# Kernel tuning notes

Measured on AMD Instinct MI355X. Metric: run time of the kernel, lower is better.

Reference implementation:

```python
import jax, jax.numpy as jnp
import numpy as np

DIM = 384
B = 256
EPS = 1e-5


def _conv_replicate(x, W, pad):
    # x: [B,C,H,W], W: [O,I,kh,kw]; replicate (edge) padding then VALID conv
    x = jnp.pad(x, ((0, 0), (0, 0), (pad, pad), (pad, pad)), mode='edge')
    return jax.lax.conv_general_dilated(
        x, W, window_strides=(1, 1), padding='VALID',
        dimension_numbers=('NCHW', 'OIHW', 'NCHW'))


def _bn(x, g, b, m, v):
    scale = (g / jnp.sqrt(v + EPS))[None, :, None, None]
    return (x - m[None, :, None, None]) * scale + b[None, :, None, None]


def _clip_features(target, bbox):
    # target: [B, 576, C] -> vectorized per-sample crop + nearest resize to 12x12
    bb = bbox * 24.0
    x, y, w, h = bb[:, 0], bb[:, 1], bb[:, 2], bb[:, 3]
    l = (w + h) / 2
    l = jnp.sqrt((w + l) * (h + l))
    x_min = jnp.clip(jnp.ceil(x - l / 2), 0, 23).astype(jnp.int32)
    y_min = jnp.clip(jnp.ceil(y - l / 2), 0, 23).astype(jnp.int32)
    x_max = jnp.clip(jnp.trunc(x + l / 2), 0, 23).astype(jnp.int32)
    y_max = jnp.clip(jnp.trunc(y + l / 2), 0, 23).astype(jnp.int32)
    i12 = jnp.arange(12, dtype=jnp.int32)
    # nearest-neighbor source index: crop_start + floor(i * crop_size / 12)
    rows = y_min[:, None] + (i12[None, :] * (y_max - y_min)[:, None]) // 12  # [B,12]
    cols = x_min[:, None] + (i12[None, :] * (x_max - x_min)[:, None]) // 12  # [B,12]
    rows = jnp.clip(rows, 0, 23)
    cols = jnp.clip(cols, 0, 23)
    Bn, N, C = target.shape
    tflat = jnp.transpose(target, (0, 2, 1))  # [B, C, 576] (row-major 24x24)
    idx = rows[:, :, None] * 24 + cols[:, None, :]  # [B,12,12]
    idx = jnp.broadcast_to(idx.reshape(Bn, 1, 144), (Bn, C, 144))
    out = jnp.take_along_axis(tflat, idx, axis=2)  # [B, C, 144]
    return out.reshape(Bn, C, 12, 12)


def setup_inputs() -> dict:
    key = jax.random.key(0)
    ks = jax.random.split(key, 8)
    temp = jax.random.normal(ks[0], (B, 144, DIM), dtype=jnp.float32)
    target = jax.random.normal(ks[1], (B, 576, DIM), dtype=jnp.float32)
    u = jax.random.uniform(ks[2], (B, 4), dtype=jnp.float32)
    # centers in [0.3,0.7], sizes in [0.25,0.45] -> always a valid non-empty crop
    bbox = jnp.concatenate([0.3 + 0.4 * u[:, :2], 0.25 + 0.2 * u[:, 2:]], axis=1)
    W1 = jax.random.normal(ks[3], (DIM, DIM, 5, 5), dtype=jnp.float32) * 0.02
    W2 = jax.random.normal(ks[4], (DIM, DIM, 3, 3), dtype=jnp.float32) * 0.05
    g1 = jnp.ones((DIM,), jnp.float32)
    b1 = jnp.zeros((DIM,), jnp.float32)
    m1 = jax.random.normal(ks[5], (DIM,), dtype=jnp.float32) * 0.1
    v1 = jnp.ones((DIM,), jnp.float32)
    g2 = jnp.ones((DIM,), jnp.float32)
    b2 = jnp.zeros((DIM,), jnp.float32)
    m2 = jax.random.normal(ks[6], (DIM,), dtype=jnp.float32) * 0.1
    v2 = jnp.ones((DIM,), jnp.float32)
    return dict(temp=temp, target=target, bbox=bbox, W1=W1, g1=g1, b1=b1,
                m1=m1, v1=v1, W2=W2, g2=g2, b2=b2, m2=m2, v2=v2)


def reference(temp, target, bbox, W1, g1, b1, m1, v1, W2, g2, b2, m2, v2):
    ta = _clip_features(target, bbox)  # [B, C, 12, 12]
    h1 = jax.nn.leaky_relu(_bn(_conv_replicate(ta, W1, 2), g1, b1, m1, v1), 0.01)
    h2 = jax.nn.leaky_relu(_bn(_conv_replicate(h1, W2, 1), g2, b2, m2, v2), 0.01)
    Bn, N, C = temp.shape
    t = jnp.transpose(temp, (0, 2, 1)).reshape(Bn, C, 12, 12)
    out = (t + h2).reshape(Bn, C, 144)
    return jnp.transpose(out, (0, 2, 1))  # [B, 144, C]
```

## Files before the change

### kernel.cpp

```cpp
#include <hip/hip_runtime.h>
#include <math.h>

#define NBATCH 256
#define CDIM   384

typedef __attribute__((ext_vector_type(4))) float  f32x4;
typedef __attribute__((ext_vector_type(8))) __bf16 bf16x8;
typedef __attribute__((ext_vector_type(4))) __bf16 bf16x4;

__device__ __forceinline__ void load16(const void* g, void* l) {
    __builtin_amdgcn_global_load_lds(
        (const __attribute__((address_space(1))) void*)g,
        (__attribute__((address_space(3))) void*)l, 16, 0, 0);
}

__global__ __launch_bounds__(256) void gather_bf16(
    const float* __restrict__ target,
    const float* __restrict__ bbox,
    __bf16* __restrict__ ta)
{
    const int b = blockIdx.x, t = threadIdx.x;
    __shared__ int pos[144];

    if (t < 144) {
        const float bx0 = bbox[b * 4 + 0] * 24.f;
        const float by0 = bbox[b * 4 + 1] * 24.f;
        const float bw  = bbox[b * 4 + 2] * 24.f;
        const float bh  = bbox[b * 4 + 3] * 24.f;
        const float l0 = (bw + bh) * 0.5f;
        const float l  = sqrtf((bw + l0) * (bh + l0));
        const int xmin = (int)fminf(fmaxf(ceilf (bx0 - l * 0.5f), 0.f), 23.f);
        const int ymin = (int)fminf(fmaxf(ceilf (by0 - l * 0.5f), 0.f), 23.f);
        const int xmax = (int)fminf(fmaxf(truncf(bx0 + l * 0.5f), 0.f), 23.f);
        const int ymax = (int)fminf(fmaxf(truncf(by0 + l * 0.5f), 0.f), 23.f);
        const int i = t / 12, j = t % 12;
        int r = ymin + (i * (ymax - ymin)) / 12;
        int c = xmin + (j * (xmax - xmin)) / 12;
        r = min(max(r, 0), 23);
        c = min(max(c, 0), 23);
        pos[t] = r * 24 + c;
    }
    __syncthreads();

    const float* tb  = target + (size_t)b * 576 * 384;
    __bf16*      tab = ta     + (size_t)b * 144 * 384;
    for (int idx = t; idx < 144 * 96; idx += 256) {
        const int p = idx / 96, c4 = idx - p * 96;
        const float4 v = *(const float4*)&tb[(size_t)pos[p] * 384 + c4 * 4];
        bf16x4 o = { (__bf16)v.x, (__bf16)v.y, (__bf16)v.z, (__bf16)v.w };
        *(bf16x4*)&tab[(size_t)p * 384 + c4 * 4] = o;
    }
}

template <int TAPS>
__global__ __launch_bounds__(256) void prep_w(
    const float* __restrict__ W, __bf16* __restrict__ Wt)
{
    const int K = TAPS * 384;
    __shared__ float ws[TAPS * 384];
    const int oc = blockIdx.x;
    const float* src = W + (size_t)oc * K;
    for (int i = threadIdx.x; i < K; i += 256) ws[i] = src[i];
    __syncthreads();
    __bf16* dst = Wt + (size_t)oc * K;
    for (int i = threadIdx.x; i < K; i += 256) {
        const int tap = i / 384;
        const int ic  = i - tap * 384;
        dst[i] = (__bf16)ws[ic * TAPS + tap];
    }
}

template <int TAPS, int KW, int PAD, bool RESID>
__global__ __launch_bounds__(256, 3) void conv_mfma(
    const __bf16* __restrict__ A,
    const __bf16* __restrict__ Wt,
    const float* __restrict__ gg, const float* __restrict__ bb,
    const float* __restrict__ mm, const float* __restrict__ vv,
    const float* __restrict__ temp,
    void* __restrict__ outp)
{
    const int K  = TAPS * 384;
    const int IT = TAPS * 12;
    const int m0 = blockIdx.x * 128;
    const int n0 = blockIdx.y * 128;
    const int t  = threadIdx.x;
    const int lane  = t & 63, w = t >> 6;
    const int wm    = (w & 1) * 64, wn = (w >> 1) * 64;
    const int col16 = lane & 15,  quad = lane >> 4;

    __shared__ __bf16 As0[128 * 32], As1[128 * 32], As2[128 * 32];
    __shared__ __bf16 Bs0[128 * 32], Bs1[128 * 32], Bs2[128 * 32];

    const int r0   = t >> 2, slot = t & 3;
    const int kg   = slot ^ ((r0 >> 1) & 3);
    const int mrow0 = m0 + r0, mrow1 = m0 + r0 + 64;
    const int b0 = mrow0 / 144, p0 = mrow0 - b0 * 144;
    const int b1 = mrow1 / 144, p1 = mrow1 - b1 * 144;
    const int y0 = p0 / 12, x0 = p0 - y0 * 12;
    const int y1 = p1 / 12, x1 = p1 - y1 * 12;
    const __bf16* Ab0 = A + (size_t)b0 * 144 * 384 + kg * 8;
    const __bf16* Ab1 = A + (size_t)b1 * 144 * 384 + kg * 8;

    int offA[4], offB[4];
#pragma unroll
    for (int mi = 0; mi < 4; ++mi) {
        const int r = wm + mi * 16 + col16;
        offA[mi] = r * 32 + (quad ^ ((r >> 1) & 3)) * 8;
    }
#pragma unroll
    for (int ni = 0; ni < 4; ++ni) {
        const int r = wn + ni * 16 + col16;
        offB[ni] = r * 32 + (quad ^ ((r >> 1) & 3)) * 8;
    }

    f32x4 acc[4][4];
#pragma unroll
    for (int mi = 0; mi < 4; ++mi)
#pragma unroll
        for (int ni = 0; ni < 4; ++ni)
            acc[mi][ni] = (f32x4){0.f, 0.f, 0.f, 0.f};

    int jn = 0, tapn = 0, next = 0;
    const __bf16* aT0;
    const __bf16* aT1;
    {
        const int sy0 = min(max(y0 - PAD, 0), 11), sx0 = min(max(x0 - PAD, 0), 11);
        const int sy1 = min(max(y1 - PAD, 0), 11), sx1 = min(max(x1 - PAD, 0), 11);
        aT0 = Ab0 + (size_t)(sy0 * 12 + sx0) * 384;
        aT1 = Ab1 + (size_t)(sy1 * 12 + sx1) * 384;
    }
    const __bf16* bT0 = Wt + (size_t)(n0 + r0)      * K + kg * 8;
    const __bf16* bT1 = Wt + (size_t)(n0 + r0 + 64) * K + kg * 8;

    auto issue = [&](__bf16* SA, __bf16* SB) {
        load16(aT0 + jn * 32, &SA[t * 8]);
        load16(aT1 + jn * 32, &SA[(t + 256) * 8]);
        load16(bT0 + jn * 32, &SB[t * 8]);
        load16(bT1 + jn * 32, &SB[(t + 256) * 8]);
    };
    auto advance = [&]() {
        if (++jn == 12) {
            jn = 0;
            ++tapn;
            if (tapn < TAPS) {
                const int ky = tapn / KW - PAD, kx = tapn % KW - PAD;
                const int sy0 = min(max(y0 + ky, 0), 11), sx0 = min(max(x0 + kx, 0), 11);
                const int sy1 = min(max(y1 + ky, 0), 11), sx1 = min(max(x1 + kx, 0), 11);
                aT0 = Ab0 + (size_t)(sy0 * 12 + sx0) * 384;
                aT1 = Ab1 + (size_t)(sy1 * 12 + sx1) * 384;
                bT0 += 384;
                bT1 += 384;
            }
        }
    };
    auto step = [&](const __bf16* SA, const __bf16* SB,
                    __bf16* NA, __bf16* NB_, bool last) {
        if (last) asm volatile("s_waitcnt vmcnt(0)" ::: "memory");
        else      asm volatile("s_waitcnt vmcnt(4)" ::: "memory");
        __builtin_amdgcn_s_barrier();
        __builtin_amdgcn_sched_barrier(0);
        if (next < IT) { issue(NA, NB_); advance(); ++next; }
        bf16x8 av[4], bv[4];
#pragma unroll
        for (int mi = 0; mi < 4; ++mi) av[mi] = *(const bf16x8*)&SA[offA[mi]];
#pragma unroll
        for (int ni = 0; ni < 4; ++ni) bv[ni] = *(const bf16x8*)&SB[offB[ni]];
        __builtin_amdgcn_s_setprio(1);
#pragma unroll
        for (int mi = 0; mi < 4; ++mi)
#pragma unroll
            for (int ni = 0; ni < 4; ++ni)
                acc[mi][ni] = __builtin_amdgcn_mfma_f32_16x16x32_bf16(
                    av[mi], bv[ni], acc[mi][ni], 0, 0, 0);
        __builtin_amdgcn_s_setprio(0);
    };

    issue(As0, Bs0); advance(); ++next;
    issue(As1, Bs1); advance(); ++next;

    for (int it3 = 0; it3 < IT; it3 += 3) {
        step(As0, Bs0, As2, Bs2, it3 + 1 == IT);
        step(As1, Bs1, As0, Bs0, it3 + 2 == IT);
        step(As2, Bs2, As1, Bs1, it3 + 3 == IT);
    }

#pragma unroll
    for (int ni = 0; ni < 4; ++ni) {
        const int gn = n0 + wn + ni * 16 + col16;
        const float scale = gg[gn] * rsqrtf(vv[gn] + 1e-5f);
        const float shift = bb[gn] - mm[gn] * scale;
        if (!RESID) {
            __bf16* h1 = (__bf16*)outp;
#pragma unroll
            for (int mi = 0; mi < 4; ++mi) {
                const int gm = m0 + wm + mi * 16 + quad * 4;
#pragma unroll
                for (int r = 0; r < 4; ++r) {
                    float v = acc[mi][ni][r] * scale + shift;
                    v = (v >= 0.f) ? v : 0.01f * v;
                    h1[(size_t)(gm + r) * 384 + gn] = (__bf16)v;
                }
            }
        } else {
            float* outF = (float*)outp;
#pragma unroll
            for (int mi = 0; mi < 4; ++mi) {
                const int gm = m0 + wm + mi * 16 + quad * 4;
#pragma unroll
                for (int r = 0; r < 4; ++r) {
                    float v = acc[mi][ni][r] * scale + shift;
                    v = (v >= 0.f) ? v : 0.01f * v;
                    outF[(size_t)(gm + r) * 384 + gn] =
                        temp[(size_t)(gm + r) * 384 + gn] + v;
                }
            }
        }
    }
}

extern "C" void kernel_launch(void* const* d_in, const int* in_sizes, int n_in,
                              void* d_out, int out_size, void* d_ws, size_t ws_size,
                              hipStream_t stream) {
    const float* temp   = (const float*)d_in[0];
    const float* target = (const float*)d_in[1];
    const float* bbox   = (const float*)d_in[2];
    const float* W1     = (const float*)d_in[3];
    const float* g1     = (const float*)d_in[4];
    const float* b1     = (const float*)d_in[5];
    const float* m1     = (const float*)d_in[6];
    const float* v1     = (const float*)d_in[7];
    const float* W2     = (const float*)d_in[8];
    const float* g2     = (const float*)d_in[9];
    const float* b2     = (const float*)d_in[10];
    const float* m2     = (const float*)d_in[11];
    const float* v2     = (const float*)d_in[12];
    float* out = (float*)d_out;

    __bf16* ta  = (__bf16*)d_ws;
    __bf16* h1  = ta  + (size_t)NBATCH * 144 * CDIM;
    __bf16* Wt1 = h1  + (size_t)NBATCH * 144 * CDIM;
    __bf16* Wt2 = Wt1 + (size_t)CDIM * 25 * CDIM;

    prep_w<25><<<dim3(CDIM), dim3(256), 0, stream>>>(W1, Wt1);
    prep_w<9><<<dim3(CDIM), dim3(256), 0, stream>>>(W2, Wt2);
    gather_bf16<<<dim3(NBATCH), dim3(256), 0, stream>>>(target, bbox, ta);

    conv_mfma<25, 5, 2, false><<<dim3(288, 3), dim3(256), 0, stream>>>(
        ta, Wt1, g1, b1, m1, v1, nullptr, (void*)h1);
    conv_mfma<9, 3, 1, true><<<dim3(288, 3), dim3(256), 0, stream>>>(
        h1, Wt2, g2, b2, m2, v2, temp, (void*)out);
}
```

Baseline: 835.4 us.

## Enlarge conv GEMM tile to 256x128 and remap blocks for XCD locality

Each block of the implicit-GEMM convolutions now computes a 256x128 output tile instead of 128x128. Each wave holds an 8x4 grid of MFMA accumulators, so more MFMAs run per LDS byte loaded and per barrier. A linear block index is also permuted so that consecutive work items land on the same XCD, which should improve L2 reuse of the A and weight tiles. The cost is higher register and LDS use (occupancy hint lowered to 2 blocks per SIMD) and half as many blocks (432), which may leave the 256 CUs less evenly loaded.

```diff
diff --git a/kernel.cpp b/kernel.cpp
--- a/kernel.cpp
+++ b/kernel.cpp
@@ -71,7 +71,7 @@
 }
 
 template <int TAPS, int KW, int PAD, bool RESID>
-__global__ __launch_bounds__(256, 3) void conv_mfma(
+__global__ __launch_bounds__(256, 2) void conv_mfma(
     const __bf16* __restrict__ A,
     const __bf16* __restrict__ Wt,
     const float* __restrict__ gg, const float* __restrict__ bb,
@@ -81,29 +81,38 @@
 {
     const int K  = TAPS * 384;
     const int IT = TAPS * 12;
-    const int m0 = blockIdx.x * 128;
-    const int n0 = blockIdx.y * 128;
+
+    const int l    = blockIdx.x + 144 * blockIdx.y;
+    const int work = (l & 7) * 54 + (l >> 3);
+    const int wx   = work % 144, wy = work / 144;
+    const int m0   = wx * 256;
+    const int n0   = wy * 128;
+
     const int t  = threadIdx.x;
     const int lane  = t & 63, w = t >> 6;
-    const int wm    = (w & 1) * 64, wn = (w >> 1) * 64;
+    const int wm    = (w & 1) * 128, wn = (w >> 1) * 64;
     const int col16 = lane & 15,  quad = lane >> 4;
 
-    __shared__ __bf16 As0[128 * 32], As1[128 * 32], As2[128 * 32];
+    __shared__ __bf16 As0[256 * 32], As1[256 * 32], As2[256 * 32];
     __shared__ __bf16 Bs0[128 * 32], Bs1[128 * 32], Bs2[128 * 32];
 
     const int r0   = t >> 2, slot = t & 3;
     const int kg   = slot ^ ((r0 >> 1) & 3);
-    const int mrow0 = m0 + r0, mrow1 = m0 + r0 + 64;
-    const int b0 = mrow0 / 144, p0 = mrow0 - b0 * 144;
-    const int b1 = mrow1 / 144, p1 = mrow1 - b1 * 144;
-    const int y0 = p0 / 12, x0 = p0 - y0 * 12;
-    const int y1 = p1 / 12, x1 = p1 - y1 * 12;
-    const __bf16* Ab0 = A + (size_t)b0 * 144 * 384 + kg * 8;
-    const __bf16* Ab1 = A + (size_t)b1 * 144 * 384 + kg * 8;
-
-    int offA[4], offB[4];
-#pragma unroll
-    for (int mi = 0; mi < 4; ++mi) {
+
+    int yq[4], xq[4];
+    const __bf16* Abq[4];
+#pragma unroll
+    for (int q = 0; q < 4; ++q) {
+        const int mrow = m0 + r0 + 64 * q;
+        const int b = mrow / 144, p = mrow - b * 144;
+        yq[q] = p / 12;
+        xq[q] = p - yq[q] * 12;
+        Abq[q] = A + (size_t)b * 144 * 384 + kg * 8;
+    }
+
+    int offA[8], offB[4];
+#pragma unroll
+    for (int mi = 0; mi < 8; ++mi) {
         const int r = wm + mi * 16 + col16;
         offA[mi] = r * 32 + (quad ^ ((r >> 1) & 3)) * 8;
     }
@@ -113,30 +122,29 @@
         offB[ni] = r * 32 + (quad ^ ((r >> 1) & 3)) * 8;
     }
 
-    f32x4 acc[4][4];
-#pragma unroll
-    for (int mi = 0; mi < 4; ++mi)
+    f32x4 acc[8][4];
+#pragma unroll
+    for (int mi = 0; mi < 8; ++mi)
 #pragma unroll
         for (int ni = 0; ni < 4; ++ni)
             acc[mi][ni] = (f32x4){0.f, 0.f, 0.f, 0.f};
 
     int jn = 0, tapn = 0, next = 0;
-    const __bf16* aT0;
-    const __bf16* aT1;
-    {
-        const int sy0 = min(max(y0 - PAD, 0), 11), sx0 = min(max(x0 - PAD, 0), 11);
-        const int sy1 = min(max(y1 - PAD, 0), 11), sx1 = min(max(x1 - PAD, 0), 11);
-        aT0 = Ab0 + (size_t)(sy0 * 12 + sx0) * 384;
-        aT1 = Ab1 + (size_t)(sy1 * 12 + sx1) * 384;
+    const __bf16* aT[4];
+#pragma unroll
+    for (int q = 0; q < 4; ++q) {
+        const int sy = min(max(yq[q] - PAD, 0), 11), sx = min(max(xq[q] - PAD, 0), 11);
+        aT[q] = Abq[q] + (size_t)(sy * 12 + sx) * 384;
     }
     const __bf16* bT0 = Wt + (size_t)(n0 + r0)      * K + kg * 8;
     const __bf16* bT1 = Wt + (size_t)(n0 + r0 + 64) * K + kg * 8;
 
     auto issue = [&](__bf16* SA, __bf16* SB) {
-        load16(aT0 + jn * 32, &SA[t * 8]);
-        load16(aT1 + jn * 32, &SA[(t + 256) * 8]);
+#pragma unroll
+        for (int q = 0; q < 4; ++q)
+            load16(aT[q] + jn * 32, &SA[t * 8 + q * 2048]);
         load16(bT0 + jn * 32, &SB[t * 8]);
-        load16(bT1 + jn * 32, &SB[(t + 256) * 8]);
+        load16(bT1 + jn * 32, &SB[t * 8 + 2048]);
     };
     auto advance = [&]() {
         if (++jn == 12) {
@@ -144,10 +152,12 @@
             ++tapn;
             if (tapn < TAPS) {
                 const int ky = tapn / KW - PAD, kx = tapn % KW - PAD;
-                const int sy0 = min(max(y0 + ky, 0), 11), sx0 = min(max(x0 + kx, 0), 11);
-                const int sy1 = min(max(y1 + ky, 0), 11), sx1 = min(max(x1 + kx, 0), 11);
-                aT0 = Ab0 + (size_t)(sy0 * 12 + sx0) * 384;
-                aT1 = Ab1 + (size_t)(sy1 * 12 + sx1) * 384;
+#pragma unroll
+                for (int q = 0; q < 4; ++q) {
+                    const int sy = min(max(yq[q] + ky, 0), 11);
+                    const int sx = min(max(xq[q] + kx, 0), 11);
+                    aT[q] = Abq[q] + (size_t)(sy * 12 + sx) * 384;
+                }
                 bT0 += 384;
                 bT1 += 384;
             }
@@ -156,18 +166,18 @@
     auto step = [&](const __bf16* SA, const __bf16* SB,
                     __bf16* NA, __bf16* NB_, bool last) {
         if (last) asm volatile("s_waitcnt vmcnt(0)" ::: "memory");
-        else      asm volatile("s_waitcnt vmcnt(4)" ::: "memory");
+        else      asm volatile("s_waitcnt vmcnt(6)" ::: "memory");
         __builtin_amdgcn_s_barrier();
         __builtin_amdgcn_sched_barrier(0);
         if (next < IT) { issue(NA, NB_); advance(); ++next; }
-        bf16x8 av[4], bv[4];
-#pragma unroll
-        for (int mi = 0; mi < 4; ++mi) av[mi] = *(const bf16x8*)&SA[offA[mi]];
+        bf16x8 av[8], bv[4];
 #pragma unroll
         for (int ni = 0; ni < 4; ++ni) bv[ni] = *(const bf16x8*)&SB[offB[ni]];
+#pragma unroll
+        for (int mi = 0; mi < 8; ++mi) av[mi] = *(const bf16x8*)&SA[offA[mi]];
         __builtin_amdgcn_s_setprio(1);
 #pragma unroll
-        for (int mi = 0; mi < 4; ++mi)
+        for (int mi = 0; mi < 8; ++mi)
 #pragma unroll
             for (int ni = 0; ni < 4; ++ni)
                 acc[mi][ni] = __builtin_amdgcn_mfma_f32_16x16x32_bf16(
@@ -192,7 +202,7 @@
         if (!RESID) {
             __bf16* h1 = (__bf16*)outp;
 #pragma unroll
-            for (int mi = 0; mi < 4; ++mi) {
+            for (int mi = 0; mi < 8; ++mi) {
                 const int gm = m0 + wm + mi * 16 + quad * 4;
 #pragma unroll
                 for (int r = 0; r < 4; ++r) {
@@ -204,7 +214,7 @@
         } else {
             float* outF = (float*)outp;
 #pragma unroll
-            for (int mi = 0; mi < 4; ++mi) {
+            for (int mi = 0; mi < 8; ++mi) {
                 const int gm = m0 + wm + mi * 16 + quad * 4;
 #pragma unroll
                 for (int r = 0; r < 4; ++r) {
@@ -245,8 +255,8 @@
     prep_w<9><<<dim3(CDIM), dim3(256), 0, stream>>>(W2, Wt2);
     gather_bf16<<<dim3(NBATCH), dim3(256), 0, stream>>>(target, bbox, ta);
 
-    conv_mfma<25, 5, 2, false><<<dim3(288, 3), dim3(256), 0, stream>>>(
+    conv_mfma<25, 5, 2, false><<<dim3(144, 3), dim3(256), 0, stream>>>(
         ta, Wt1, g1, b1, m1, v1, nullptr, (void*)h1);
-    conv_mfma<9, 3, 1, true><<<dim3(288, 3), dim3(256), 0, stream>>>(
+    conv_mfma<9, 3, 1, true><<<dim3(144, 3), dim3(256), 0, stream>>>(
         h1, Wt2, g2, b2, m2, v2, temp, (void*)out);
 }
```

Measured after the change: 954.6 us. 1.14x slower.
